# Kernel tuning notes

Measured on AMD Instinct MI355X. Metric: run time of the kernel, lower is better.

## Reference

```python
import jax, jax.numpy as jnp
import numpy as np

HIDDEN = 128
STATE = 64
ACTION = 16
D_IO = STATE + ACTION  # 80
BATCH = 4096
SEQ_LEN = 512


def setup_inputs() -> dict:
    key = jax.random.key(0)
    ks = jax.random.split(key, 7)
    s = 1.0 / np.sqrt(HIDDEN)
    return {
        "quantized_hn": jax.random.normal(ks[0], (BATCH, HIDDEN), jnp.float32),
        "W_ih": jax.random.uniform(ks[1], (4 * HIDDEN, D_IO), jnp.float32, -s, s),
        "W_hh": jax.random.uniform(ks[2], (4 * HIDDEN, HIDDEN), jnp.float32, -s, s),
        "b_ih": jax.random.uniform(ks[3], (4 * HIDDEN,), jnp.float32, -s, s),
        "b_hh": jax.random.uniform(ks[4], (4 * HIDDEN,), jnp.float32, -s, s),
        "W_fc": jax.random.uniform(ks[5], (D_IO, HIDDEN), jnp.float32, -s, s),
        "b_fc": jax.random.uniform(ks[6], (D_IO,), jnp.float32, -s, s),
        "seq_len": SEQ_LEN,
    }


def reference(quantized_hn, W_ih, W_hh, b_ih, b_hh, W_fc, b_fc, seq_len):
    B, H = quantized_hn.shape
    D = W_fc.shape[0]

    def step(carry, _):
        h, c, x = carry  # h,c: (B,H); x: (B,D)
        # PyTorch LSTM gate order: i, f, g, o
        gates = x @ W_ih.T + b_ih + h @ W_hh.T + b_hh  # (B, 4H)
        i, f, g, o = jnp.split(gates, 4, axis=-1)
        c_new = jax.nn.sigmoid(f) * c + jax.nn.sigmoid(i) * jnp.tanh(g)
        h_new = jax.nn.sigmoid(o) * jnp.tanh(c_new)
        y = h_new @ W_fc.T + b_fc  # (B, D) -> fed back as next input
        return (h_new, c_new, y), y

    h0 = quantized_hn
    c0 = jnp.zeros((B, H), quantized_hn.dtype)
    x0 = jnp.zeros((B, D), quantized_hn.dtype)
    _, ys = jax.lax.scan(step, (h0, c0, x0), None, length=seq_len)
    return jnp.transpose(ys, (1, 0, 2))  # (B, seq_len, D)
```

## Files before the change

### kernel.cpp

```cpp
#include <hip/hip_runtime.h>

typedef __bf16 bf16_t;
typedef __bf16 bf16x4 __attribute__((ext_vector_type(4)));
typedef __bf16 bf16x8 __attribute__((ext_vector_type(8)));
typedef float  f32x4  __attribute__((ext_vector_type(4)));

#define HID    128
#define DIO    80
#define G4     512
#define TSTEP  512
#define BB     16
#define NBATCH 4096
#define NBLK   (NBATCH / BB)
#define HSTR   136

#define NL2E  -1.4426950408889634f
#define P2L2E  2.8853900817779268f

__device__ bf16_t g_weff_frags[128 * 512];
__device__ bf16_t g_whh_frags[128 * 512];
__device__ bf16_t g_wfc_frags[20 * 512];
__device__ float  g_weff[G4 * HID];
__device__ float  g_beff[G4];
__device__ float  g_b1[G4];

__global__ void k_weff(const float* __restrict__ W_ih, const float* __restrict__ W_hh,
                       const float* __restrict__ b_ih, const float* __restrict__ b_hh,
                       const float* __restrict__ W_fc, const float* __restrict__ b_fc) {
  int gid = blockIdx.x * blockDim.x + threadIdx.x;
  int g = gid >> 7, k = gid & 127;
  float sc = ((g >> 7) == 2) ? P2L2E : NL2E;
  float acc = W_hh[g * HID + k];
#pragma unroll 8
  for (int d = 0; d < DIO; ++d)
    acc = fmaf(W_ih[g * DIO + d], W_fc[d * HID + k], acc);
  g_weff[g * HID + k] = acc * sc;
  if (k == 0) {
    float bb = b_ih[g] + b_hh[g];
    g_b1[g] = bb * sc;
    float be = bb;
    for (int d = 0; d < DIO; ++d) be = fmaf(W_ih[g * DIO + d], b_fc[d], be);
    g_beff[g] = be * sc;
  }
}

__global__ void k_frag(const float* __restrict__ W_hh, const float* __restrict__ W_fc) {
  int tile = blockIdx.x;
  int lane = threadIdx.x;
  int c = lane & 15, q = lane >> 4;
  if (tile < 128) {
    int gtile = tile >> 2, kt = tile & 3;
    int n = gtile * 16 + c;
#pragma unroll
    for (int j = 0; j < 8; ++j)
      g_weff_frags[tile * 512 + lane * 8 + j] = (bf16_t)g_weff[n * HID + kt * 32 + q * 8 + j];
  } else if (tile < 256) {
    int t2 = tile - 128;
    int gtile = t2 >> 2, kt = t2 & 3;
    int n = gtile * 16 + c;
    float sc = ((n >> 7) == 2) ? P2L2E : NL2E;
#pragma unroll
    for (int j = 0; j < 8; ++j)
      g_whh_frags[t2 * 512 + lane * 8 + j] = (bf16_t)(W_hh[n * HID + kt * 32 + q * 8 + j] * sc);
  } else {
    int t2 = tile - 256;
    int yt = t2 >> 2, kt = t2 & 3;
    int n = yt * 16 + c;
#pragma unroll
    for (int j = 0; j < 8; ++j)
      g_wfc_frags[t2 * 512 + lane * 8 + j] = (bf16_t)W_fc[n * HID + kt * 32 + q * 8 + j];
  }
}

__global__ __launch_bounds__(512, 2) void k_lstm(const float* __restrict__ h0,
                                                 const float* __restrict__ b_fc,
                                                 float* __restrict__ out) {
  __shared__ __align__(16) bf16_t hbuf[2][BB * HSTR];
  const int tid = threadIdx.x;
  const int lane = tid & 63;
  const int w = tid >> 6;
  const int c = lane & 15, q = lane >> 4;
  const int b0 = blockIdx.x * BB;

  for (int i = tid; i < BB * HID; i += 512) {
    int r = i >> 7, k = i & 127;
    hbuf[0][r * HSTR + k] = (bf16_t)h0[(long)(b0 + r) * HID + k];
  }

  bf16x8 Wy[4];
  f32x4  ybias;
  if (w < 5) {
#pragma unroll
    for (int kt = 0; kt < 4; ++kt)
      Wy[kt] = *(const bf16x8*)&g_wfc_frags[(w * 4 + kt) * 512 + lane * 8];
#pragma unroll
    for (int r = 0; r < 4; ++r) ybias[r] = b_fc[w * 16 + q * 4 + r];
  }

  bf16x8 Wg[4][4];
  f32x4  bias[4];
  auto load_wg = [&](const bf16_t* frags, const float* bsrc) {
#pragma unroll
    for (int G = 0; G < 4; ++G) {
      int gtile = G * 8 + w;
#pragma unroll
      for (int r = 0; r < 4; ++r) bias[G][r] = bsrc[gtile * 16 + q * 4 + r];
#pragma unroll
      for (int kt = 0; kt < 4; ++kt)
        Wg[G][kt] = *(const bf16x8*)&frags[(gtile * 4 + kt) * 512 + lane * 8];
    }
  };

  f32x4 cst = (f32x4){0, 0, 0, 0};
  bf16x8 hf[4];

  __syncthreads();
#pragma unroll
  for (int kt = 0; kt < 4; ++kt)
    hf[kt] = *(const bf16x8*)&hbuf[0][c * HSTR + kt * 32 + q * 8];

  float* outp = out + (long)(b0 + c) * TSTEP * DIO + w * 16 + q * 4;

  if (((tid >> 6) & 1) == 0) __builtin_amdgcn_s_setprio(1);

  auto step = [&](int t) {
    f32x4 acc[4];
#pragma unroll
    for (int G = 0; G < 4; ++G)
      acc[G] = __builtin_amdgcn_mfma_f32_16x16x32_bf16(Wg[G][0], hf[0], bias[G], 0, 0, 0);
#pragma unroll
    for (int kt = 1; kt < 4; ++kt)
#pragma unroll
      for (int G = 0; G < 4; ++G)
        acc[G] = __builtin_amdgcn_mfma_f32_16x16x32_bf16(Wg[G][kt], hf[kt], acc[G], 0, 0, 0);

    const int buf = t & 1;
    bf16x4 hv;
#pragma unroll
    for (int r = 0; r < 4; ++r) {
      float Ei = __builtin_amdgcn_exp2f(acc[0][r]);
      float Ef = __builtin_amdgcn_exp2f(acc[1][r]);
      float Eg = __builtin_amdgcn_exp2f(acc[2][r]);
      float Eo = __builtin_amdgcn_exp2f(acc[3][r]);
      float ai = 1.0f + Ei, af = 1.0f + Ef, ag = 1.0f + Eg;
      float P1 = ai * ag;
      float R  = __builtin_amdgcn_rcpf(P1 * af);
      float fs = P1 * R;
      float tg = __builtin_fmaf(Eg, P2L2E, -P2L2E);
      float term = tg * af * R;
      float cn = __builtin_fmaf(fs, cst[r], term);
      cst[r] = cn;
      float cc = fminf(cn, 80.0f);
      float Ec = __builtin_amdgcn_exp2f(cc);
      float R2 = __builtin_amdgcn_rcpf((1.0f + Eo) * (1.0f + Ec));
      hv[r] = (bf16_t)((Ec - 1.0f) * R2);
    }
    *(bf16x4*)&hbuf[buf][c * HSTR + w * 16 + q * 4] = hv;
    __syncthreads();
#pragma unroll
    for (int kt = 0; kt < 4; ++kt)
      hf[kt] = *(const bf16x8*)&hbuf[buf][c * HSTR + kt * 32 + q * 8];

    if (w < 5) {
      f32x4 ya = __builtin_amdgcn_mfma_f32_16x16x32_bf16(Wy[0], hf[0], ybias, 0, 0, 0);
#pragma unroll
      for (int kt = 1; kt < 4; ++kt)
        ya = __builtin_amdgcn_mfma_f32_16x16x32_bf16(Wy[kt], hf[kt], ya, 0, 0, 0);
      *(f32x4*)outp = ya;
      outp += DIO;
    }
  };

  load_wg(g_whh_frags, g_b1);
  step(1);
  load_wg(g_weff_frags, g_beff);
  for (int t = 2; t <= TSTEP; ++t) step(t);
}

extern "C" void kernel_launch(void* const* d_in, const int* in_sizes, int n_in,
                              void* d_out, int out_size, void* d_ws, size_t ws_size,
                              hipStream_t stream) {
  const float* h0   = (const float*)d_in[0];
  const float* W_ih = (const float*)d_in[1];
  const float* W_hh = (const float*)d_in[2];
  const float* b_ih = (const float*)d_in[3];
  const float* b_hh = (const float*)d_in[4];
  const float* W_fc = (const float*)d_in[5];
  const float* b_fc = (const float*)d_in[6];
  float* out = (float*)d_out;

  k_weff<<<256, 256, 0, stream>>>(W_ih, W_hh, b_ih, b_hh, W_fc, b_fc);
  k_frag<<<276, 64, 0, stream>>>(W_hh, W_fc);
  k_lstm<<<NBLK, 512, 0, stream>>>(h0, b_fc, out);
}
```

Before: 962.0 us.

## Double-buffer h fragments and defer y projection to overlap with next step

Splits the h fragment registers into two ping-pong sets and manually unrolls the recurrence by two. Each step now emits the output projection for the previous step's h from the current-step fragments after the barrier, so the y MFMAs no longer sit directly on the critical dependency after the LDS reload. The cell update is also reordered to fold the reciprocal multiply into one final product. This costs extra registers for the second fragment set and a tail projection after the loop, which may affect occupancy.

```diff
diff --git a/kernel.cpp b/kernel.cpp
--- a/kernel.cpp
+++ b/kernel.cpp
@@ -72,6 +72,9 @@
   }
 }
 
+__device__ __forceinline__ float fexp2(float x) { return __builtin_amdgcn_exp2f(x); }
+__device__ __forceinline__ float frcp(float x)  { return __builtin_amdgcn_rcpf(x); }
+
 __global__ __launch_bounds__(512, 2) void k_lstm(const float* __restrict__ h0,
                                                  const float* __restrict__ b_fc,
                                                  float* __restrict__ out) {
@@ -112,69 +115,80 @@
   };
 
   f32x4 cst = (f32x4){0, 0, 0, 0};
-  bf16x8 hf[4];
+  bf16x8 hfA[4], hfB[4];
 
   __syncthreads();
 #pragma unroll
   for (int kt = 0; kt < 4; ++kt)
-    hf[kt] = *(const bf16x8*)&hbuf[0][c * HSTR + kt * 32 + q * 8];
+    hfA[kt] = *(const bf16x8*)&hbuf[0][c * HSTR + kt * 32 + q * 8];
 
   float* outp = out + (long)(b0 + c) * TSTEP * DIO + w * 16 + q * 4;
 
   if (((tid >> 6) & 1) == 0) __builtin_amdgcn_s_setprio(1);
 
-  auto step = [&](int t) {
-    f32x4 acc[4];
-#pragma unroll
-    for (int G = 0; G < 4; ++G)
-      acc[G] = __builtin_amdgcn_mfma_f32_16x16x32_bf16(Wg[G][0], hf[0], bias[G], 0, 0, 0);
+#define ITER(CUR, NXT, BUF, EMIT)                                                      \
+  do {                                                                                 \
+    f32x4 acc[4];                                                                      \
+    _Pragma("unroll")                                                                  \
+    for (int G = 0; G < 4; ++G)                                                        \
+      acc[G] = __builtin_amdgcn_mfma_f32_16x16x32_bf16(Wg[G][0], CUR[0], bias[G], 0, 0, 0); \
+    _Pragma("unroll")                                                                  \
+    for (int kt = 1; kt < 4; ++kt)                                                     \
+      _Pragma("unroll")                                                                \
+      for (int G = 0; G < 4; ++G)                                                      \
+        acc[G] = __builtin_amdgcn_mfma_f32_16x16x32_bf16(Wg[G][kt], CUR[kt], acc[G], 0, 0, 0); \
+    bf16x4 hv;                                                                         \
+    _Pragma("unroll")                                                                  \
+    for (int r = 0; r < 4; ++r) {                                                      \
+      float Ei = fexp2(acc[0][r]);                                           \
+      float Ef = fexp2(acc[1][r]);                                           \
+      float Eg = fexp2(acc[2][r]);                                           \
+      float Eo = fexp2(acc[3][r]);                                           \
+      float ai = 1.0f + Ei, af = 1.0f + Ef, ag = 1.0f + Eg;                            \
+      float P1 = ai * ag;                                                              \
+      float R  = frcp(P1 * af);                                                        \
+      float tg = __builtin_fmaf(Eg, P2L2E, -P2L2E);                     \
+      float m2 = tg * af;                                                              \
+      float u  = __builtin_fmaf(P1, cst[r], m2);                                       \
+      float cn = u * R;                            \
+      cst[r] = cn;                                                                     \
+      float cc = fminf(cn, 80.0f);                            \
+      float Ec = fexp2(cc);                                                  \
+      float R2 = frcp((1.0f + Eo) * (1.0f + Ec));                                      \
+      hv[r] = (bf16_t)((Ec - 1.0f) * R2);                          \
+    }                                                                                  \
+    *(bf16x4*)&hbuf[BUF][c * HSTR + w * 16 + q * 4] = hv;                              \
+    __syncthreads();                                                                   \
+    _Pragma("unroll")                                                                  \
+    for (int kt = 0; kt < 4; ++kt)                                                     \
+      NXT[kt] = *(const bf16x8*)&hbuf[BUF][c * HSTR + kt * 32 + q * 8];                \
+    if (EMIT && w < 5) {  \
+      f32x4 ya = __builtin_amdgcn_mfma_f32_16x16x32_bf16(Wy[0], CUR[0], ybias, 0, 0, 0); \
+      _Pragma("unroll")                                                                \
+      for (int kt = 1; kt < 4; ++kt)                                                   \
+        ya = __builtin_amdgcn_mfma_f32_16x16x32_bf16(Wy[kt], CUR[kt], ya, 0, 0, 0);    \
+      *(f32x4*)outp = ya;                                                              \
+      outp += DIO;                                                                     \
+    }                                                                                  \
+  } while (0)
+
+  load_wg(g_whh_frags, g_b1);
+  ITER(hfA, hfB, 1, false);
+  load_wg(g_weff_frags, g_beff);
+  for (int p = 0; p < 255; ++p) {
+    ITER(hfB, hfA, 0, true);
+    ITER(hfA, hfB, 1, true);
+  }
+  ITER(hfB, hfA, 0, true);
+
+  if (w < 5) {
+    f32x4 ya = __builtin_amdgcn_mfma_f32_16x16x32_bf16(Wy[0], hfA[0], ybias, 0, 0, 0);
 #pragma unroll
     for (int kt = 1; kt < 4; ++kt)
-#pragma unroll
-      for (int G = 0; G < 4; ++G)
-        acc[G] = __builtin_amdgcn_mfma_f32_16x16x32_bf16(Wg[G][kt], hf[kt], acc[G], 0, 0, 0);
-
-    const int buf = t & 1;
-    bf16x4 hv;
-#pragma unroll
-    for (int r = 0; r < 4; ++r) {
-      float Ei = __builtin_amdgcn_exp2f(acc[0][r]);
-      float Ef = __builtin_amdgcn_exp2f(acc[1][r]);
-      float Eg = __builtin_amdgcn_exp2f(acc[2][r]);
-      float Eo = __builtin_amdgcn_exp2f(acc[3][r]);
-      float ai = 1.0f + Ei, af = 1.0f + Ef, ag = 1.0f + Eg;
-      float P1 = ai * ag;
-      float R  = __builtin_amdgcn_rcpf(P1 * af);
-      float fs = P1 * R;
-      float tg = __builtin_fmaf(Eg, P2L2E, -P2L2E);
-      float term = tg * af * R;
-      float cn = __builtin_fmaf(fs, cst[r], term);
-      cst[r] = cn;
-      float cc = fminf(cn, 80.0f);
-      float Ec = __builtin_amdgcn_exp2f(cc);
-      float R2 = __builtin_amdgcn_rcpf((1.0f + Eo) * (1.0f + Ec));
-      hv[r] = (bf16_t)((Ec - 1.0f) * R2);
-    }
-    *(bf16x4*)&hbuf[buf][c * HSTR + w * 16 + q * 4] = hv;
-    __syncthreads();
-#pragma unroll
-    for (int kt = 0; kt < 4; ++kt)
-      hf[kt] = *(const bf16x8*)&hbuf[buf][c * HSTR + kt * 32 + q * 8];
-
-    if (w < 5) {
-      f32x4 ya = __builtin_amdgcn_mfma_f32_16x16x32_bf16(Wy[0], hf[0], ybias, 0, 0, 0);
-#pragma unroll
-      for (int kt = 1; kt < 4; ++kt)
-        ya = __builtin_amdgcn_mfma_f32_16x16x32_bf16(Wy[kt], hf[kt], ya, 0, 0, 0);
-      *(f32x4*)outp = ya;
-      outp += DIO;
-    }
-  };
-
-  load_wg(g_whh_frags, g_b1);
-  step(1);
-  load_wg(g_weff_frags, g_beff);
-  for (int t = 2; t <= TSTEP; ++t) step(t);
+      ya = __builtin_amdgcn_mfma_f32_16x16x32_bf16(Wy[kt], hfA[kt], ya, 0, 0, 0);
+    *(f32x4*)outp = ya;
+  }
+#undef ITER
 }
 
 extern "C" void kernel_launch(void* const* d_in, const int* in_sizes, int n_in,
```

Result: faster. 931.7 us (-3.1%).
